# Performance work log

Measured on AMD Instinct MI355X. Metric: run time of the kernel, lower is better.

## Reference

```python
import jax, jax.numpy as jnp
import numpy as np

L, D_MODEL, D_INNER, DT_RANK, D_STATE, D_CONV, VOCAB = 4, 768, 1536, 48, 16, 4, 32000
B, S = 1, 1024


def rmsnorm(x, w, eps=1e-5):
    return x * jax.lax.rsqrt(jnp.mean(x * x, axis=-1, keepdims=True) + eps) * w


def causal_depthwise_conv(x, w, b):
    # x: [B,S,D]; w: [D,1,K] (torch Conv1d groups=D weight layout); causal left-pad K-1
    y = jax.lax.conv_general_dilated(
        x.transpose(0, 2, 1), w, window_strides=(1,), padding=[(D_CONV - 1, 0)],
        dimension_numbers=('NCH', 'OIH', 'NCH'), feature_group_count=D_INNER)
    return y.transpose(0, 2, 1) + b


def selective_scan(u, dt, A, Bm, Cm, Dv):
    # Faithful to the source: A_delta = exp(dt (x) A), clamp(min=-20) is a no-op on exp output
    A_delta = jnp.clip(jnp.exp(jnp.einsum('bld,dn->bldn', dt, A)), -20.0, None)
    B_delta_u = jnp.einsum('bld,bld,bln->bldn', dt, u, Bm)
    shifted = jnp.pad(A_delta[:, 1:], ((0, 0), (1, 0), (0, 0), (0, 0)))
    A_cum = jnp.exp(jnp.cumsum(shifted, axis=1))
    h = B_delta_u / (A_cum + 1e-12)
    y = jnp.einsum('bldn,bln->bld', jnp.cumsum(h, axis=1) * A_cum, Cm)
    return y + u * Dv


def setup_inputs() -> dict:
    key = jax.random.key(0)
    ks = jax.random.split(key, 8)
    return {
        'tokens': jax.random.randint(ks[0], (B, S), 0, VOCAB),
        'embedding': jax.random.normal(ks[1], (VOCAB, D_MODEL), jnp.float32) * 0.02,
        'norm_w': jnp.ones((L, D_MODEL), jnp.float32),
        'in_proj_w': jax.random.normal(ks[2], (L, 2 * D_INNER, D_MODEL), jnp.float32) * 0.02,
        'conv_w': jax.random.normal(ks[3], (L, D_INNER, 1, D_CONV), jnp.float32) * 0.2,
        'conv_b': jnp.zeros((L, D_INNER), jnp.float32),
        'x_proj_w': jax.random.normal(ks[4], (L, DT_RANK + 2 * D_STATE, D_INNER), jnp.float32) * 0.02,
        'dt_proj_w': jax.random.normal(ks[5], (L, D_INNER, DT_RANK), jnp.float32) * 0.001,
        'dt_proj_b': jnp.full((L, D_INNER), 5.0, jnp.float32),  # delta~5 keeps exp(cumsum(exp(dt*A))) finite
        'A_log': jnp.tile(jnp.log(jnp.arange(1, D_STATE + 1, dtype=jnp.float32)), (L, D_INNER, 1)),
        'D_skip': jnp.ones((L, D_INNER), jnp.float32),
        'out_proj_w': jax.random.normal(ks[6], (L, D_MODEL, D_INNER), jnp.float32) * 0.02,
        'final_norm_w': jnp.ones((D_MODEL,), jnp.float32),
    }


def reference(tokens, embedding, norm_w, in_proj_w, conv_w, conv_b, x_proj_w,
              dt_proj_w, dt_proj_b, A_log, D_skip, out_proj_w, final_norm_w):
    x = embedding[tokens]  # [B,S,d_model]
    for i in range(L):
        h = rmsnorm(x, norm_w[i])
        xz = h @ in_proj_w[i].T                      # [B,S,2*d_inner]
        xi, res = xz[..., :D_INNER], xz[..., D_INNER:]
        xi = jax.nn.silu(causal_depthwise_conv(xi, conv_w[i], conv_b[i]))
        proj = xi @ x_proj_w[i].T                    # [B,S,dt_rank+2*d_state]
        dt = jax.nn.softplus(proj[..., :DT_RANK] @ dt_proj_w[i].T + dt_proj_b[i])
        Bm = proj[..., DT_RANK:DT_RANK + D_STATE]
        Cm = proj[..., DT_RANK + D_STATE:]
        A = -jnp.exp(A_log[i])                       # [d_inner, d_state]
        y = selective_scan(xi, dt, A, Bm, Cm, D_skip[i])
        x = x + (y * jax.nn.silu(res)) @ out_proj_w[i].T
    return rmsnorm(x, final_norm_w) @ embedding.T    # tied LM head: [B,S,vocab]
```

## Files before the change

### kernel.cpp

```cpp
#include <hip/hip_runtime.h>
#include <hip/hip_bf16.h>
#include <cmath>

namespace {

constexpr int kL      = 4;
constexpr int kDModel = 768;
constexpr int kDInner = 1536;
constexpr int kDtRank = 48;
constexpr int kDState = 16;
constexpr int kDConv  = 4;
constexpr int kSeq    = 1024;
constexpr int kPLd    = 96;
constexpr int kPB     = 128;
constexpr int kVocab  = 32000;
constexpr int kCH     = 64;
constexpr int kNCH    = kSeq / kCH;
constexpr int kDN     = kDInner * kDState;

using short8 = __attribute__((ext_vector_type(8))) short;
using f32x4  = __attribute__((ext_vector_type(4))) float;

__device__ __forceinline__ float silu_f(float v) {
    return v / (1.f + __expf(-v));
}

__device__ __forceinline__ void split_bf16(float v, __hip_bfloat16& hi, __hip_bfloat16& lo) {
    hi = __float2bfloat16(v);
    lo = __float2bfloat16(v - __bfloat162float(hi));
}

__global__ void __launch_bounds__(256) f2b_kernel(
    const float* __restrict__ src, __hip_bfloat16* __restrict__ dst, int n) {
    int i = (blockIdx.x * 256 + threadIdx.x) * 4;
    const int stride = gridDim.x * 256 * 4;
    for (; i + 3 < n; i += stride) {
        const float4 v = *reinterpret_cast<const float4*>(src + i);
        dst[i + 0] = __float2bfloat16(v.x);
        dst[i + 1] = __float2bfloat16(v.y);
        dst[i + 2] = __float2bfloat16(v.z);
        dst[i + 3] = __float2bfloat16(v.w);
    }
}

__global__ void __launch_bounds__(256) split3_kernel(
    const float* __restrict__ src, int ldsrc, int rows, int cols,
    __hip_bfloat16* __restrict__ dst, int rowsPad) {
    const int idx = blockIdx.x * 256 + threadIdx.x;
    if (idx >= rowsPad * cols) return;
    const int r = idx / cols, c = idx % cols;
    const float v = (r < rows) ? src[(size_t)r * ldsrc + c] : 0.f;
    __hip_bfloat16 hi, lo;
    split_bf16(v, hi, lo);
    __hip_bfloat16* row = dst + (size_t)r * 3 * cols;
    row[c] = hi; row[cols + c] = hi; row[2 * cols + c] = lo;
}

__global__ void __launch_bounds__(256) split3x_kernel(
    const float* __restrict__ src, __hip_bfloat16* __restrict__ dst) {
    const int idx = blockIdx.x * 256 + threadIdx.x;
    if (idx >= kL * kPB * kDInner) return;
    const int layer = idx / (kPB * kDInner);
    const int rem   = idx % (kPB * kDInner);
    const int r = rem / kDInner, c = rem % kDInner;
    const float v = (r < kDtRank + 2 * kDState)
        ? src[(size_t)layer * (kDtRank + 2 * kDState) * kDInner + (size_t)r * kDInner + c]
        : 0.f;
    __hip_bfloat16 hi, lo;
    split_bf16(v, hi, lo);
    __hip_bfloat16* row = dst + ((size_t)layer * kPB + r) * 3 * kDInner;
    row[c] = hi; row[kDInner + c] = hi; row[2 * kDInner + c] = lo;
}

__global__ void __launch_bounds__(256) embed_kernel(
    const int* __restrict__ tokens, const float* __restrict__ emb,
    float* __restrict__ x) {
    const int s = blockIdx.x;
    const int t = tokens[s];
    const float* src = emb + (size_t)t * kDModel;
    float* dst = x + (size_t)s * kDModel;
    for (int d = threadIdx.x; d < kDModel; d += blockDim.x) dst[d] = src[d];
}

template <bool SPLIT>
__global__ void __launch_bounds__(256) rmsnorm_kernel(
    const float* __restrict__ x, const float* __restrict__ w,
    __hip_bfloat16* __restrict__ out) {
    const int s = blockIdx.x;
    const float* row = x + (size_t)s * kDModel;
    float ss = 0.f;
    for (int d = threadIdx.x; d < kDModel; d += blockDim.x) {
        const float v = row[d];
        ss = fmaf(v, v, ss);
    }
    #pragma unroll
    for (int m = 32; m; m >>= 1) ss += __shfl_xor(ss, m);
    __shared__ float red[4];
    if ((threadIdx.x & 63) == 0) red[threadIdx.x >> 6] = ss;
    __syncthreads();
    const float total = red[0] + red[1] + red[2] + red[3];
    const float scale = rsqrtf(total / (float)kDModel + 1e-5f);
    __hip_bfloat16* dst = out + (size_t)s * (SPLIT ? 3 * kDModel : kDModel);
    for (int d = threadIdx.x; d < kDModel; d += blockDim.x) {
        const float v = row[d] * scale * w[d];
        if (SPLIT) {
            __hip_bfloat16 hi, lo;
            split_bf16(v, hi, lo);
            dst[d] = hi; dst[kDModel + d] = lo; dst[2 * kDModel + d] = hi;
        } else {
            dst[d] = __float2bfloat16(v);
        }
    }
}

template <int BM, int BN, int KSPLIT>
__global__ void __launch_bounds__(256) mfma_gemm(
    const __hip_bfloat16* __restrict__ A, int lda,
    const __hip_bfloat16* __restrict__ B, int ldb,
    float* __restrict__ C, int ldc,
    int N, int K, size_t partStride) {
    constexpr int BK = 32;
    static_assert(BM == 128 && BN == 128, "staging assumes 128x128");
    __shared__ unsigned short As[3][BM * BK];
    __shared__ unsigned short Bs[3][BN * BK];
    const int tid  = threadIdx.x;
    const int lane = tid & 63;

    const int nwg = gridDim.x * gridDim.y;
    int bid = blockIdx.y * gridDim.x + blockIdx.x;
    {
        const int q = nwg >> 3, r = nwg & 7;
        const int xcd = bid & 7, pos = bid >> 3;
        bid = (xcd < r ? xcd * (q + 1) : r * (q + 1) + (xcd - r) * q) + pos;
    }
    const int m0 = (bid % gridDim.x) * BM;
    const int n0 = (bid / gridDim.x) * BN;

    const int Kp = K / KSPLIT;
    const int kbeg = (KSPLIT > 1) ? blockIdx.z * Kp : 0;
    float* Cw = (KSPLIT > 1) ? C + (size_t)blockIdx.z * partStride : C;
    constexpr int WM = BM / 2, WN = BN / 2;
    constexpr int MR = WM / 16, NR = WN / 16;
    const int wave = tid >> 6;
    const int wm = (wave >> 1) * WM, wn = (wave & 1) * WN;
    const int l15 = lane & 15, l4 = lane >> 4;
    f32x4 acc[MR][NR] = {};

    auto stage = [&](int buf, int k0) {
        #pragma unroll
        for (int i = 0; i < 2; ++i) {
            const int idx = tid + i * 256;
            const int r = idx >> 2, qv = idx & 3;
            const int qs = qv ^ ((r >> 1) & 3);
            __builtin_amdgcn_global_load_lds(
                (const __attribute__((address_space(1))) void*)(A + (size_t)(m0 + r) * lda + k0 + qs * 8),
                (__attribute__((address_space(3))) void*)(&As[buf][(idx - lane) * 8]),
                16, 0, 0);
        }
        #pragma unroll
        for (int i = 0; i < 2; ++i) {
            const int idx = tid + i * 256;
            const int r = idx >> 2, qv = idx & 3;
            const int qs = qv ^ ((r >> 1) & 3);
            __builtin_amdgcn_global_load_lds(
                (const __attribute__((address_space(1))) void*)(B + (size_t)(n0 + r) * ldb + k0 + qs * 8),
                (__attribute__((address_space(3))) void*)(&Bs[buf][(idx - lane) * 8]),
                16, 0, 0);
        }
    };

    const int nt = Kp / BK;
    stage(0, kbeg);
    if (nt > 1) stage(1, kbeg + BK);
    for (int t = 0; t < nt; ++t) {
        const int cur = t % 3;
        if (t + 2 < nt) stage((t + 2) % 3, kbeg + (t + 2) * BK);
        const int rem = nt - 1 - t;
        if (rem >= 2)      asm volatile("s_waitcnt vmcnt(8)" ::: "memory");
        else if (rem == 1) asm volatile("s_waitcnt vmcnt(4)" ::: "memory");
        else               asm volatile("s_waitcnt vmcnt(0)" ::: "memory");
        __builtin_amdgcn_s_barrier();

        short8 af[MR], bfv[NR];
        #pragma unroll
        for (int mi = 0; mi < MR; ++mi) {
            const int R = wm + mi * 16 + l15;
            af[mi] = *reinterpret_cast<const short8*>(&As[cur][(R * 4 + (l4 ^ ((R >> 1) & 3))) * 8]);
        }
        #pragma unroll
        for (int ni = 0; ni < NR; ++ni) {
            const int R = wn + ni * 16 + l15;
            bfv[ni] = *reinterpret_cast<const short8*>(&Bs[cur][(R * 4 + (l4 ^ ((R >> 1) & 3))) * 8]);
        }
        #pragma unroll
        for (int mi = 0; mi < MR; ++mi)
            #pragma unroll
            for (int ni = 0; ni < NR; ++ni)
                acc[mi][ni] = __builtin_amdgcn_mfma_f32_16x16x32_bf16(
                    af[mi], bfv[ni], acc[mi][ni], 0, 0, 0);

        asm volatile("s_waitcnt lgkmcnt(0)" ::: "memory");
        __builtin_amdgcn_s_barrier();
    }

    #pragma unroll
    for (int mi = 0; mi < MR; ++mi) {
        const int mrow = m0 + wm + mi * 16 + l4 * 4;
        #pragma unroll
        for (int ni = 0; ni < NR; ++ni) {
            const int ncol = n0 + wn + ni * 16 + l15;
            if (ncol >= N) continue;
            #pragma unroll
            for (int r = 0; r < 4; ++r)
                Cw[(size_t)(mrow + r) * ldc + ncol] = acc[mi][ni][r];
        }
    }
}

template <int NP, bool ADD>
__global__ void __launch_bounds__(256) reduce_parts(
    const float* __restrict__ parts, size_t stride,
    float* __restrict__ dst, int count) {
    const int i = (blockIdx.x * 256 + threadIdx.x) * 4;
    if (i >= count) return;
    float4 s = *reinterpret_cast<const float4*>(parts + i);
    #pragma unroll
    for (int p = 1; p < NP; ++p) {
        const float4 v = *reinterpret_cast<const float4*>(parts + (size_t)p * stride + i);
        s.x += v.x; s.y += v.y; s.z += v.z; s.w += v.w;
    }
    float4* d = reinterpret_cast<float4*>(dst + i);
    if (ADD) {
        float4 o = *d;
        o.x += s.x; o.y += s.y; o.z += s.z; o.w += s.w;
        *d = o;
    } else {
        *d = s;
    }
}

__global__ void __launch_bounds__(256) dt_kernel(
    const float* __restrict__ proj, const float* __restrict__ dtw,
    const float* __restrict__ bias, float* __restrict__ dt) {
    __shared__ float sw[kDtRank][257];
    const int tid = threadIdx.x;
    const int n0 = blockIdx.x * 256;
    const int m0 = blockIdx.y * 8;
    for (int idx = tid; idx < 256 * kDtRank; idx += 256) {
        const int nn = idx / kDtRank, k = idx % kDtRank;
        sw[k][nn] = dtw[(size_t)(n0 + nn) * kDtRank + k];
    }
    __syncthreads();
    const int n = n0 + tid;
    const float b = bias[n];
    #pragma unroll
    for (int mi = 0; mi < 8; ++mi) {
        const float* pr = proj + (size_t)(m0 + mi) * kPLd;
        float acc = b;
        #pragma unroll
        for (int k = 0; k < kDtRank; ++k)
            acc = fmaf(pr[k], sw[k][tid], acc);
        acc = (acc > 20.f) ? acc : log1pf(__expf(acc));
        dt[(size_t)(m0 + mi) * kDInner + n] = acc;
    }
}

__global__ void __launch_bounds__(256) conv_silu_kernel(
    const float* __restrict__ p0, const float* __restrict__ p1,
    const float* __restrict__ cw, const float* __restrict__ cb,
    float* __restrict__ xi, __hip_bfloat16* __restrict__ xi2) {
    const int s = blockIdx.x;
    const int d = blockIdx.y * 256 + threadIdx.x;
    float acc = cb[d];
    #pragma unroll
    for (int k = 0; k < kDConv; ++k) {
        const int sl = s - (kDConv - 1) + k;
        if (sl >= 0) {
            const size_t off = (size_t)sl * (2 * kDInner) + d;
            acc = fmaf(p0[off] + p1[off], cw[d * kDConv + k], acc);
        }
    }
    const float v = silu_f(acc);
    xi[(size_t)s * kDInner + d] = v;
    __hip_bfloat16 hi, lo;
    split_bf16(v, hi, lo);
    __hip_bfloat16* row = xi2 + (size_t)s * 3 * kDInner;
    row[d] = hi; row[kDInner + d] = lo; row[2 * kDInner + d] = hi;
}

__global__ void __launch_bounds__(256) scan_part1(
    const float* __restrict__ dt, const float* __restrict__ u,
    const float* __restrict__ proj, const float* __restrict__ A_log,
    float* __restrict__ P, float* __restrict__ S) {
    __shared__ float sdt[kCH][16], su[kCH][16], sB[kCH][16];
    const int tid = threadIdx.x;
    const int n = tid & 15, dl = tid >> 4;
    const int d0 = blockIdx.x * 16;
    const int l0 = blockIdx.y * kCH;
    for (int idx = tid; idx < kCH * 16; idx += 256) {
        const int r = idx >> 4, c = idx & 15;
        sdt[r][c] = dt[(size_t)(l0 + r) * kDInner + d0 + c];
        su [r][c] = u [(size_t)(l0 + r) * kDInner + d0 + c];
        sB [r][c] = proj[(size_t)(l0 + r) * kPLd + kDtRank + c];
    }
    __syncthreads();
    const int d = d0 + dl;
    const float Adn = -__expf(A_log[d * kDState + n]);
    float state = 0.f, sumA = 0.f;
    #pragma unroll 8
    for (int l = 0; l < kCH; ++l) {
        const float dtv = sdt[l][dl];
        const float adelta = __expf(dtv * Adn);
        const float mult = __expf(adelta);
        state = fmaf(state, mult, dtv * su[l][dl] * sB[l][n]);
        sumA += adelta;
    }
    const int dn = d * kDState + n;
    P[(size_t)blockIdx.y * kDN + dn] = __expf(sumA);
    S[(size_t)blockIdx.y * kDN + dn] = state;
}

__global__ void __launch_bounds__(256) scan_part2(
    const float* __restrict__ dt, const float* __restrict__ u,
    const float* __restrict__ proj, const float* __restrict__ A_log,
    const float* __restrict__ D_skip, const float* __restrict__ P,
    const float* __restrict__ S, float* __restrict__ y) {
    __shared__ float sdt[kCH][16], su[kCH][16], sB[kCH][16], sC[kCH][16];
    __shared__ float sy[kCH][16];
    const int tid = threadIdx.x;
    const int n = tid & 15, dl = tid >> 4;
    const int d0 = blockIdx.x * 16;
    const int l0 = blockIdx.y * kCH;
    for (int idx = tid; idx < kCH * 16; idx += 256) {
        const int r = idx >> 4, c = idx & 15;
        sdt[r][c] = dt[(size_t)(l0 + r) * kDInner + d0 + c];
        su [r][c] = u [(size_t)(l0 + r) * kDInner + d0 + c];
        sB [r][c] = proj[(size_t)(l0 + r) * kPLd + kDtRank + c];
        sC [r][c] = proj[(size_t)(l0 + r) * kPLd + kDtRank + kDState + c];
    }
    const int dn = d0 * kDState + tid;
    float state = 0.f;
    for (int jj = 0; jj < (int)blockIdx.y; ++jj) {
        const size_t idx = (size_t)jj * kDN + dn;
        state = fmaf(state, P[idx], S[idx]);
    }
    __syncthreads();
    const int d = d0 + dl;
    const float Adn = -__expf(A_log[d * kDState + n]);
    const float Dv  = D_skip[d];
    for (int l = 0; l < kCH; ++l) {
        const float dtv = sdt[l][dl];
        const float uv  = su[l][dl];
        const float mult = __expf(__expf(dtv * Adn));
        state = fmaf(state, mult, dtv * uv * sB[l][n]);
        float contrib = state * sC[l][n];
        contrib += __shfl_xor(contrib, 8);
        contrib += __shfl_xor(contrib, 4);
        contrib += __shfl_xor(contrib, 2);
        contrib += __shfl_xor(contrib, 1);
        if (n == 0) sy[l][dl] = fmaf(uv, Dv, contrib);
    }
    __syncthreads();
    for (int idx = tid; idx < kCH * 16; idx += 256) {
        const int r = idx >> 4, c = idx & 15;
        y[(size_t)(l0 + r) * kDInner + d0 + c] = sy[r][c];
    }
}

__global__ void __launch_bounds__(256) mul_silu_kernel(
    const float* __restrict__ y, const float* __restrict__ p0,
    const float* __restrict__ p1, __hip_bfloat16* __restrict__ g2) {
    const int s = blockIdx.x;
    const int d = blockIdx.y * 256 + threadIdx.x;
    const size_t off = (size_t)s * (2 * kDInner) + kDInner + d;
    const float res = p0[off] + p1[off];
    const float v = y[(size_t)s * kDInner + d] * silu_f(res);
    __hip_bfloat16 hi, lo;
    split_bf16(v, hi, lo);
    __hip_bfloat16* row = g2 + (size_t)s * 3 * kDInner;
    row[d] = hi; row[kDInner + d] = lo; row[2 * kDInner + d] = hi;
}

}

extern "C" void kernel_launch(void* const* d_in, const int* in_sizes, int n_in,
                              void* d_out, int out_size, void* d_ws, size_t ws_size,
                              hipStream_t stream) {
    const int*   tokens       = (const int*)d_in[0];
    const float* embedding    = (const float*)d_in[1];
    const float* norm_w       = (const float*)d_in[2];
    const float* in_proj_w    = (const float*)d_in[3];
    const float* conv_w       = (const float*)d_in[4];
    const float* conv_b       = (const float*)d_in[5];
    const float* x_proj_w     = (const float*)d_in[6];
    const float* dt_proj_w    = (const float*)d_in[7];
    const float* dt_proj_b    = (const float*)d_in[8];
    const float* A_log        = (const float*)d_in[9];
    const float* D_skip       = (const float*)d_in[10];
    const float* out_proj_w   = (const float*)d_in[11];
    const float* final_norm_w = (const float*)d_in[12];
    float* out = (float*)d_out;

    constexpr int K3m = 3 * kDModel;
    constexpr int K3i = 3 * kDInner;

    char* ws = (char*)d_ws;
    auto alloc = [&](size_t bytes) { char* p = ws; ws += (bytes + 255) & ~(size_t)255; return p; };
    float* x    = (float*)alloc((size_t)kSeq * kDModel * 4);
    float* xi   = (float*)alloc((size_t)kSeq * kDInner * 4);
    float* proj = (float*)alloc((size_t)kSeq * kPLd * 4);
    float* dt   = (float*)alloc((size_t)kSeq * kDInner * 4);
    float* y    = (float*)alloc((size_t)kSeq * kDInner * 4);
    float* scanP  = (float*)alloc((size_t)kNCH * kDN * 4);
    float* scanS  = (float*)alloc((size_t)kNCH * kDN * 4);
    float* partsXZ = (float*)alloc((size_t)2 * kSeq * 2 * kDInner * 4);
    float* partsP  = (float*)alloc((size_t)24 * kSeq * kPLd * 4);
    float* partsO  = (float*)alloc((size_t)6 * kSeq * kDModel * 4);
    __hip_bfloat16* h_bf   = (__hip_bfloat16*)alloc((size_t)kSeq * kDModel * 2);
    __hip_bfloat16* h2     = (__hip_bfloat16*)alloc((size_t)kSeq * K3m * 2);
    __hip_bfloat16* xi2    = (__hip_bfloat16*)alloc((size_t)kSeq * K3i * 2);
    __hip_bfloat16* g2     = (__hip_bfloat16*)alloc((size_t)kSeq * K3i * 2);
    __hip_bfloat16* emb_bf = (__hip_bfloat16*)alloc((size_t)kVocab * kDModel * 2);
    __hip_bfloat16* inw2   = (__hip_bfloat16*)alloc((size_t)kL * 2 * kDInner * K3m * 2);
    __hip_bfloat16* outw2  = (__hip_bfloat16*)alloc((size_t)kL * kDModel * K3i * 2);
    __hip_bfloat16* xw2    = (__hip_bfloat16*)alloc((size_t)kL * kPB * K3i * 2);

    f2b_kernel<<<4096, 256, 0, stream>>>(embedding, emb_bf, kVocab * kDModel);
    split3_kernel<<<(kL * 2 * kDInner * kDModel + 255) / 256, 256, 0, stream>>>(
        in_proj_w, kDModel, kL * 2 * kDInner, kDModel, inw2, kL * 2 * kDInner);
    split3_kernel<<<(kL * kDModel * kDInner + 255) / 256, 256, 0, stream>>>(
        out_proj_w, kDInner, kL * kDModel, kDInner, outw2, kL * kDModel);
    split3x_kernel<<<(kL * kPB * kDInner + 255) / 256, 256, 0, stream>>>(
        x_proj_w, xw2);

    embed_kernel<<<kSeq, 256, 0, stream>>>(tokens, embedding, x);

    for (int i = 0; i < kL; ++i) {
        rmsnorm_kernel<true><<<kSeq, 256, 0, stream>>>(x, norm_w + (size_t)i * kDModel, h2);

        mfma_gemm<128, 128, 2><<<dim3(kSeq / 128, 2 * kDInner / 128, 2), 256, 0, stream>>>(
            h2, K3m, inw2 + (size_t)i * 2 * kDInner * K3m, K3m,
            partsXZ, 2 * kDInner, 2 * kDInner, K3m, (size_t)kSeq * 2 * kDInner);

        conv_silu_kernel<<<dim3(kSeq, kDInner / 256), 256, 0, stream>>>(
            partsXZ, partsXZ + (size_t)kSeq * 2 * kDInner,
            conv_w + (size_t)i * kDInner * kDConv, conv_b + (size_t)i * kDInner,
            xi, xi2);

        mfma_gemm<128, 128, 24><<<dim3(kSeq / 128, 1, 24), 256, 0, stream>>>(
            xi2, K3i, xw2 + (size_t)i * kPB * K3i, K3i,
            partsP, kPLd, kPLd, K3i, (size_t)kSeq * kPLd);
        reduce_parts<24, false><<<(kSeq * kPLd / 4 + 255) / 256, 256, 0, stream>>>(
            partsP, (size_t)kSeq * kPLd, proj, kSeq * kPLd);

        dt_kernel<<<dim3(kDInner / 256, kSeq / 8), 256, 0, stream>>>(
            proj, dt_proj_w + (size_t)i * kDInner * kDtRank,
            dt_proj_b + (size_t)i * kDInner, dt);

        const float* A_l = A_log + (size_t)i * kDInner * kDState;
        scan_part1<<<dim3(kDInner / 16, kNCH), 256, 0, stream>>>(
            dt, xi, proj, A_l, scanP, scanS);
        scan_part2<<<dim3(kDInner / 16, kNCH), 256, 0, stream>>>(
            dt, xi, proj, A_l, D_skip + (size_t)i * kDInner, scanP, scanS, y);

        mul_silu_kernel<<<dim3(kSeq, kDInner / 256), 256, 0, stream>>>(
            y, partsXZ, partsXZ + (size_t)kSeq * 2 * kDInner, g2);

        mfma_gemm<128, 128, 6><<<dim3(kSeq / 128, kDModel / 128, 6), 256, 0, stream>>>(
            g2, K3i, outw2 + (size_t)i * kDModel * K3i, K3i,
            partsO, kDModel, kDModel, K3i, (size_t)kSeq * kDModel);
        reduce_parts<6, true><<<(kSeq * kDModel / 4 + 255) / 256, 256, 0, stream>>>(
            partsO, (size_t)kSeq * kDModel, x, kSeq * kDModel);
    }

    rmsnorm_kernel<false><<<kSeq, 256, 0, stream>>>(x, final_norm_w, h_bf);
    mfma_gemm<128, 128, 1><<<dim3(kSeq / 128, kVocab / 128, 1), 256, 0, stream>>>(
        h_bf, kDModel, emb_bf, kDModel, out, kVocab, kVocab, kDModel, 0);
}
```

Measured before the change: 819.7 us.

## Fuse rmsnorm into embed/reduce, dt into scan, mul_silu into scan_part2; double-buffer GEMM

Merges the embedding copy with the first rmsnorm, and the out-proj split-K reduction plus residual add with the next layer's rmsnorm. The dt projection is recomputed inside both scan kernels from proj and dt_proj_w, and the gating multiply with silu and the bf16 split move into the scan_part2 epilogue. This removes several launches and the dt and y intermediate buffers. The GEMM also goes from triple to double buffering, which cuts LDS use but exposes more load latency, and dt is now computed twice per layer.

```diff
diff --git a/kernel.cpp b/kernel.cpp
--- a/kernel.cpp
+++ b/kernel.cpp
@@ -72,26 +72,21 @@
     row[c] = hi; row[kDInner + c] = hi; row[2 * kDInner + c] = lo;
 }
 
-__global__ void __launch_bounds__(256) embed_kernel(
+__global__ void __launch_bounds__(256) embed_rms_kernel(
     const int* __restrict__ tokens, const float* __restrict__ emb,
-    float* __restrict__ x) {
+    const float* __restrict__ w, float* __restrict__ x,
+    __hip_bfloat16* __restrict__ h2) {
     const int s = blockIdx.x;
     const int t = tokens[s];
     const float* src = emb + (size_t)t * kDModel;
-    float* dst = x + (size_t)s * kDModel;
-    for (int d = threadIdx.x; d < kDModel; d += blockDim.x) dst[d] = src[d];
-}
-
-template <bool SPLIT>
-__global__ void __launch_bounds__(256) rmsnorm_kernel(
-    const float* __restrict__ x, const float* __restrict__ w,
-    __hip_bfloat16* __restrict__ out) {
-    const int s = blockIdx.x;
-    const float* row = x + (size_t)s * kDModel;
+    float v[3];
     float ss = 0.f;
-    for (int d = threadIdx.x; d < kDModel; d += blockDim.x) {
-        const float v = row[d];
-        ss = fmaf(v, v, ss);
+    #pragma unroll
+    for (int j = 0; j < 3; ++j) {
+        const int d = threadIdx.x + j * 256;
+        v[j] = src[d];
+        x[(size_t)s * kDModel + d] = v[j];
+        ss = fmaf(v[j], v[j], ss);
     }
     #pragma unroll
     for (int m = 32; m; m >>= 1) ss += __shfl_xor(ss, m);
@@ -100,15 +95,54 @@
     __syncthreads();
     const float total = red[0] + red[1] + red[2] + red[3];
     const float scale = rsqrtf(total / (float)kDModel + 1e-5f);
-    __hip_bfloat16* dst = out + (size_t)s * (SPLIT ? 3 * kDModel : kDModel);
-    for (int d = threadIdx.x; d < kDModel; d += blockDim.x) {
-        const float v = row[d] * scale * w[d];
-        if (SPLIT) {
+    __hip_bfloat16* dst = h2 + (size_t)s * 3 * kDModel;
+    #pragma unroll
+    for (int j = 0; j < 3; ++j) {
+        const int d = threadIdx.x + j * 256;
+        const float hv = v[j] * scale * w[d];
+        __hip_bfloat16 hi, lo;
+        split_bf16(hv, hi, lo);
+        dst[d] = hi; dst[kDModel + d] = lo; dst[2 * kDModel + d] = hi;
+    }
+}
+
+template <bool FINAL>
+__global__ void __launch_bounds__(256) reduce_rms_kernel(
+    const float* __restrict__ parts, size_t stride,
+    const float* __restrict__ w, float* __restrict__ x,
+    __hip_bfloat16* __restrict__ out) {
+    const int s = blockIdx.x;
+    float v[3];
+    float ss = 0.f;
+    #pragma unroll
+    for (int j = 0; j < 3; ++j) {
+        const int d = threadIdx.x + j * 256;
+        const size_t off = (size_t)s * kDModel + d;
+        float acc = x[off];
+        #pragma unroll
+        for (int p = 0; p < 6; ++p) acc += parts[(size_t)p * stride + off];
+        v[j] = acc;
+        x[off] = acc;
+        ss = fmaf(acc, acc, ss);
+    }
+    #pragma unroll
+    for (int m = 32; m; m >>= 1) ss += __shfl_xor(ss, m);
+    __shared__ float red[4];
+    if ((threadIdx.x & 63) == 0) red[threadIdx.x >> 6] = ss;
+    __syncthreads();
+    const float total = red[0] + red[1] + red[2] + red[3];
+    const float scale = rsqrtf(total / (float)kDModel + 1e-5f);
+    #pragma unroll
+    for (int j = 0; j < 3; ++j) {
+        const int d = threadIdx.x + j * 256;
+        const float hv = v[j] * scale * w[d];
+        if (FINAL) {
+            out[(size_t)s * kDModel + d] = __float2bfloat16(hv);
+        } else {
             __hip_bfloat16 hi, lo;
-            split_bf16(v, hi, lo);
+            split_bf16(hv, hi, lo);
+            __hip_bfloat16* dst = out + (size_t)s * 3 * kDModel;
             dst[d] = hi; dst[kDModel + d] = lo; dst[2 * kDModel + d] = hi;
-        } else {
-            dst[d] = __float2bfloat16(v);
         }
     }
 }
@@ -121,8 +155,8 @@
     int N, int K, size_t partStride) {
     constexpr int BK = 32;
     static_assert(BM == 128 && BN == 128, "staging assumes 128x128");
-    __shared__ unsigned short As[3][BM * BK];
-    __shared__ unsigned short Bs[3][BN * BK];
+    __shared__ unsigned short As[2][BM * BK];
+    __shared__ unsigned short Bs[2][BN * BK];
     const int tid  = threadIdx.x;
     const int lane = tid & 63;
 
@@ -170,15 +204,15 @@
     };
 
     const int nt = Kp / BK;
+    int cur = 0;
     stage(0, kbeg);
-    if (nt > 1) stage(1, kbeg + BK);
     for (int t = 0; t < nt; ++t) {
-        const int cur = t % 3;
-        if (t + 2 < nt) stage((t + 2) % 3, kbeg + (t + 2) * BK);
-        const int rem = nt - 1 - t;
-        if (rem >= 2)      asm volatile("s_waitcnt vmcnt(8)" ::: "memory");
-        else if (rem == 1) asm volatile("s_waitcnt vmcnt(4)" ::: "memory");
-        else               asm volatile("s_waitcnt vmcnt(0)" ::: "memory");
+        if (t + 1 < nt) {
+            stage(cur ^ 1, kbeg + (t + 1) * BK);
+            asm volatile("s_waitcnt vmcnt(4)" ::: "memory");
+        } else {
+            asm volatile("s_waitcnt vmcnt(0)" ::: "memory");
+        }
         __builtin_amdgcn_s_barrier();
 
         short8 af[MR], bfv[NR];
@@ -201,6 +235,7 @@
 
         asm volatile("s_waitcnt lgkmcnt(0)" ::: "memory");
         __builtin_amdgcn_s_barrier();
+        cur ^= 1;
     }
 
     #pragma unroll
@@ -217,7 +252,7 @@
     }
 }
 
-template <int NP, bool ADD>
+template <int NP>
 __global__ void __launch_bounds__(256) reduce_parts(
     const float* __restrict__ parts, size_t stride,
     float* __restrict__ dst, int count) {
@@ -229,40 +264,7 @@
         const float4 v = *reinterpret_cast<const float4*>(parts + (size_t)p * stride + i);
         s.x += v.x; s.y += v.y; s.z += v.z; s.w += v.w;
     }
-    float4* d = reinterpret_cast<float4*>(dst + i);
-    if (ADD) {
-        float4 o = *d;
-        o.x += s.x; o.y += s.y; o.z += s.z; o.w += s.w;
-        *d = o;
-    } else {
-        *d = s;
-    }
-}
-
-__global__ void __launch_bounds__(256) dt_kernel(
-    const float* __restrict__ proj, const float* __restrict__ dtw,
-    const float* __restrict__ bias, float* __restrict__ dt) {
-    __shared__ float sw[kDtRank][257];
-    const int tid = threadIdx.x;
-    const int n0 = blockIdx.x * 256;
-    const int m0 = blockIdx.y * 8;
-    for (int idx = tid; idx < 256 * kDtRank; idx += 256) {
-        const int nn = idx / kDtRank, k = idx % kDtRank;
-        sw[k][nn] = dtw[(size_t)(n0 + nn) * kDtRank + k];
-    }
-    __syncthreads();
-    const int n = n0 + tid;
-    const float b = bias[n];
-    #pragma unroll
-    for (int mi = 0; mi < 8; ++mi) {
-        const float* pr = proj + (size_t)(m0 + mi) * kPLd;
-        float acc = b;
-        #pragma unroll
-        for (int k = 0; k < kDtRank; ++k)
-            acc = fmaf(pr[k], sw[k][tid], acc);
-        acc = (acc > 20.f) ? acc : log1pf(__expf(acc));
-        dt[(size_t)(m0 + mi) * kDInner + n] = acc;
-    }
+    *reinterpret_cast<float4*>(dst + i) = s;
 }
 
 __global__ void __launch_bounds__(256) conv_silu_kernel(
@@ -288,10 +290,40 @@
     row[d] = hi; row[kDInner + d] = lo; row[2 * kDInner + d] = hi;
 }
 
+
+__device__ __forceinline__ void compute_dt_tile(
+    const float* __restrict__ proj, const float* __restrict__ dtw,
+    const float* __restrict__ dtb, int l0, int d0, int tid,
+    float (*sP)[kDtRank], float (*sdtw)[kDtRank + 1], float (*sdt)[16]) {
+    for (int idx = tid; idx < kCH * kDtRank; idx += 256) {
+        const int r = idx / kDtRank, c = idx % kDtRank;
+        sP[r][c] = proj[(size_t)(l0 + r) * kPLd + c];
+    }
+    for (int idx = tid; idx < 16 * kDtRank; idx += 256) {
+        const int dd = idx / kDtRank, c = idx % kDtRank;
+        sdtw[dd][c] = dtw[(size_t)(d0 + dd) * kDtRank + c];
+    }
+    __syncthreads();
+    #pragma unroll
+    for (int e = 0; e < 4; ++e) {
+        const int idx = tid + e * 256;
+        const int r = idx >> 4, dd = idx & 15;
+        float acc = dtb[d0 + dd];
+        #pragma unroll
+        for (int k = 0; k < kDtRank; ++k)
+            acc = fmaf(sP[r][k], sdtw[dd][k], acc);
+        acc = (acc > 20.f) ? acc : log1pf(__expf(acc));
+        sdt[r][dd] = acc;
+    }
+}
+
 __global__ void __launch_bounds__(256) scan_part1(
-    const float* __restrict__ dt, const float* __restrict__ u,
-    const float* __restrict__ proj, const float* __restrict__ A_log,
+    const float* __restrict__ u, const float* __restrict__ proj,
+    const float* __restrict__ A_log, const float* __restrict__ dtw,
+    const float* __restrict__ dtb,
     float* __restrict__ P, float* __restrict__ S) {
+    __shared__ float sP[kCH][kDtRank];
+    __shared__ float sdtw[16][kDtRank + 1];
     __shared__ float sdt[kCH][16], su[kCH][16], sB[kCH][16];
     const int tid = threadIdx.x;
     const int n = tid & 15, dl = tid >> 4;
@@ -299,10 +331,10 @@
     const int l0 = blockIdx.y * kCH;
     for (int idx = tid; idx < kCH * 16; idx += 256) {
         const int r = idx >> 4, c = idx & 15;
-        sdt[r][c] = dt[(size_t)(l0 + r) * kDInner + d0 + c];
-        su [r][c] = u [(size_t)(l0 + r) * kDInner + d0 + c];
-        sB [r][c] = proj[(size_t)(l0 + r) * kPLd + kDtRank + c];
-    }
+        su[r][c] = u[(size_t)(l0 + r) * kDInner + d0 + c];
+        sB[r][c] = proj[(size_t)(l0 + r) * kPLd + kDtRank + c];
+    }
+    compute_dt_tile(proj, dtw, dtb, l0, d0, tid, sP, sdtw, sdt);
     __syncthreads();
     const int d = d0 + dl;
     const float Adn = -__expf(A_log[d * kDState + n]);
@@ -321,10 +353,14 @@
 }
 
 __global__ void __launch_bounds__(256) scan_part2(
-    const float* __restrict__ dt, const float* __restrict__ u,
-    const float* __restrict__ proj, const float* __restrict__ A_log,
-    const float* __restrict__ D_skip, const float* __restrict__ P,
-    const float* __restrict__ S, float* __restrict__ y) {
+    const float* __restrict__ u, const float* __restrict__ proj,
+    const float* __restrict__ A_log, const float* __restrict__ dtw,
+    const float* __restrict__ dtb, const float* __restrict__ D_skip,
+    const float* __restrict__ P, const float* __restrict__ S,
+    const float* __restrict__ res0, const float* __restrict__ res1,
+    __hip_bfloat16* __restrict__ g2) {
+    __shared__ float sP[kCH][kDtRank];
+    __shared__ float sdtw[16][kDtRank + 1];
     __shared__ float sdt[kCH][16], su[kCH][16], sB[kCH][16], sC[kCH][16];
     __shared__ float sy[kCH][16];
     const int tid = threadIdx.x;
@@ -333,11 +369,11 @@
     const int l0 = blockIdx.y * kCH;
     for (int idx = tid; idx < kCH * 16; idx += 256) {
         const int r = idx >> 4, c = idx & 15;
-        sdt[r][c] = dt[(size_t)(l0 + r) * kDInner + d0 + c];
-        su [r][c] = u [(size_t)(l0 + r) * kDInner + d0 + c];
-        sB [r][c] = proj[(size_t)(l0 + r) * kPLd + kDtRank + c];
-        sC [r][c] = proj[(size_t)(l0 + r) * kPLd + kDtRank + kDState + c];
-    }
+        su[r][c] = u[(size_t)(l0 + r) * kDInner + d0 + c];
+        sB[r][c] = proj[(size_t)(l0 + r) * kPLd + kDtRank + c];
+        sC[r][c] = proj[(size_t)(l0 + r) * kPLd + kDtRank + kDState + c];
+    }
+    compute_dt_tile(proj, dtw, dtb, l0, d0, tid, sP, sdtw, sdt);
     const int dn = d0 * kDState + tid;
     float state = 0.f;
     for (int jj = 0; jj < (int)blockIdx.y; ++jj) {
@@ -363,22 +399,14 @@
     __syncthreads();
     for (int idx = tid; idx < kCH * 16; idx += 256) {
         const int r = idx >> 4, c = idx & 15;
-        y[(size_t)(l0 + r) * kDInner + d0 + c] = sy[r][c];
-    }
-}
-
-__global__ void __launch_bounds__(256) mul_silu_kernel(
-    const float* __restrict__ y, const float* __restrict__ p0,
-    const float* __restrict__ p1, __hip_bfloat16* __restrict__ g2) {
-    const int s = blockIdx.x;
-    const int d = blockIdx.y * 256 + threadIdx.x;
-    const size_t off = (size_t)s * (2 * kDInner) + kDInner + d;
-    const float res = p0[off] + p1[off];
-    const float v = y[(size_t)s * kDInner + d] * silu_f(res);
-    __hip_bfloat16 hi, lo;
-    split_bf16(v, hi, lo);
-    __hip_bfloat16* row = g2 + (size_t)s * 3 * kDInner;
-    row[d] = hi; row[kDInner + d] = lo; row[2 * kDInner + d] = hi;
+        const size_t roff = (size_t)(l0 + r) * (2 * kDInner) + kDInner + d0 + c;
+        const float res = res0[roff] + res1[roff];
+        const float v = sy[r][c] * silu_f(res);
+        __hip_bfloat16 hi, lo;
+        split_bf16(v, hi, lo);
+        __hip_bfloat16* row = g2 + (size_t)(l0 + r) * 3 * kDInner;
+        row[d0 + c] = hi; row[kDInner + d0 + c] = lo; row[2 * kDInner + d0 + c] = hi;
+    }
 }
 
 }
@@ -409,8 +437,6 @@
     float* x    = (float*)alloc((size_t)kSeq * kDModel * 4);
     float* xi   = (float*)alloc((size_t)kSeq * kDInner * 4);
     float* proj = (float*)alloc((size_t)kSeq * kPLd * 4);
-    float* dt   = (float*)alloc((size_t)kSeq * kDInner * 4);
-    float* y    = (float*)alloc((size_t)kSeq * kDInner * 4);
     float* scanP  = (float*)alloc((size_t)kNCH * kDN * 4);
     float* scanS  = (float*)alloc((size_t)kNCH * kDN * 4);
     float* partsXZ = (float*)alloc((size_t)2 * kSeq * 2 * kDInner * 4);
@@ -433,11 +459,9 @@
     split3x_kernel<<<(kL * kPB * kDInner + 255) / 256, 256, 0, stream>>>(
         x_proj_w, xw2);
 
-    embed_kernel<<<kSeq, 256, 0, stream>>>(tokens, embedding, x);
+    embed_rms_kernel<<<kSeq, 256, 0, stream>>>(tokens, embedding, norm_w, x, h2);
 
     for (int i = 0; i < kL; ++i) {
-        rmsnorm_kernel<true><<<kSeq, 256, 0, stream>>>(x, norm_w + (size_t)i * kDModel, h2);
-
         mfma_gemm<128, 128, 2><<<dim3(kSeq / 128, 2 * kDInner / 128, 2), 256, 0, stream>>>(
             h2, K3m, inw2 + (size_t)i * 2 * kDInner * K3m, K3m,
             partsXZ, 2 * kDInner, 2 * kDInner, K3m, (size_t)kSeq * 2 * kDInner);
@@ -450,30 +474,31 @@
         mfma_gemm<128, 128, 24><<<dim3(kSeq / 128, 1, 24), 256, 0, stream>>>(
             xi2, K3i, xw2 + (size_t)i * kPB * K3i, K3i,
             partsP, kPLd, kPLd, K3i, (size_t)kSeq * kPLd);
-        reduce_parts<24, false><<<(kSeq * kPLd / 4 + 255) / 256, 256, 0, stream>>>(
+        reduce_parts<24><<<(kSeq * kPLd / 4 + 255) / 256, 256, 0, stream>>>(
             partsP, (size_t)kSeq * kPLd, proj, kSeq * kPLd);
 
-        dt_kernel<<<dim3(kDInner / 256, kSeq / 8), 256, 0, stream>>>(
-            proj, dt_proj_w + (size_t)i * kDInner * kDtRank,
-            dt_proj_b + (size_t)i * kDInner, dt);
-
-        const float* A_l = A_log + (size_t)i * kDInner * kDState;
+        const float* A_l  = A_log + (size_t)i * kDInner * kDState;
+        const float* dtw  = dt_proj_w + (size_t)i * kDInner * kDtRank;
+        const float* dtb  = dt_proj_b + (size_t)i * kDInner;
         scan_part1<<<dim3(kDInner / 16, kNCH), 256, 0, stream>>>(
-            dt, xi, proj, A_l, scanP, scanS);
+            xi, proj, A_l, dtw, dtb, scanP, scanS);
         scan_part2<<<dim3(kDInner / 16, kNCH), 256, 0, stream>>>(
-            dt, xi, proj, A_l, D_skip + (size_t)i * kDInner, scanP, scanS, y);
-
-        mul_silu_kernel<<<dim3(kSeq, kDInner / 256), 256, 0, stream>>>(
-            y, partsXZ, partsXZ + (size_t)kSeq * 2 * kDInner, g2);
+            xi, proj, A_l, dtw, dtb, D_skip + (size_t)i * kDInner,
+            scanP, scanS, partsXZ, partsXZ + (size_t)kSeq * 2 * kDInner, g2);
 
         mfma_gemm<128, 128, 6><<<dim3(kSeq / 128, kDModel / 128, 6), 256, 0, stream>>>(
             g2, K3i, outw2 + (size_t)i * kDModel * K3i, K3i,
             partsO, kDModel, kDModel, K3i, (size_t)kSeq * kDModel);
-        reduce_parts<6, true><<<(kSeq * kDModel / 4 + 255) / 256, 256, 0, stream>>>(
-            partsO, (size_t)kSeq * kDModel, x, kSeq * kDModel);
-    }
-
-    rmsnorm_kernel<false><<<kSeq, 256, 0, stream>>>(x, final_norm_w, h_bf);
+
+        if (i + 1 < kL) {
+            reduce_rms_kernel<false><<<kSeq, 256, 0, stream>>>(
+                partsO, (size_t)kSeq * kDModel, norm_w + (size_t)(i + 1) * kDModel, x, h2);
+        } else {
+            reduce_rms_kernel<true><<<kSeq, 256, 0, stream>>>(
+                partsO, (size_t)kSeq * kDModel, final_norm_w, x, h_bf);
+        }
+    }
+
     mfma_gemm<128, 128, 1><<<dim3(kSeq / 128, kVocab / 128, 1), 256, 0, stream>>>(
         h_bf, kDModel, emb_bf, kDModel, out, kVocab, kVocab, kDModel, 0);
 }
```

Result: no change. 810.5 us (-1.1%).
